# Performance work log

Measured on AMD Instinct MI355X. Metric: run time of the kernel, lower is better.

Reference implementation:

```python
import jax, jax.numpy as jnp
import numpy as np

HIDDEN = 1024
INTER = 4096
N_EXPERTS = 8
TOP_K = 2


def setup_inputs() -> dict:
    key = jax.random.key(0)
    ks = jax.random.split(key, 5)
    B, S = 2, 1024
    scale_h = 1.0 / np.sqrt(HIDDEN)
    scale_i = 1.0 / np.sqrt(INTER)
    return {
        "hidden_states": jax.random.normal(ks[0], (B, S, HIDDEN), dtype=jnp.float32),
        "router_w": jax.random.normal(ks[1], (N_EXPERTS, HIDDEN), dtype=jnp.float32) * scale_h,
        "gate_w": jax.random.normal(ks[2], (N_EXPERTS, INTER, HIDDEN), dtype=jnp.float32) * scale_h,
        "up_w": jax.random.normal(ks[3], (N_EXPERTS, INTER, HIDDEN), dtype=jnp.float32) * scale_h,
        "down_w": jax.random.normal(ks[4], (N_EXPERTS, HIDDEN, INTER), dtype=jnp.float32) * scale_i,
        "top_k": TOP_K,
    }


def reference(hidden_states, router_w, gate_w, up_w, down_w, top_k):
    B, S, D = hidden_states.shape
    E = router_w.shape[0]
    x = hidden_states.reshape(-1, D)              # [T, D]
    T = x.shape[0]

    router_logits = x @ router_w.T                # [T, E]
    probs = jax.nn.softmax(router_logits.astype(jnp.float32), axis=-1)
    routing_weights, selected = jax.lax.top_k(probs, top_k)   # [T, k]
    routing_weights = routing_weights.astype(x.dtype)

    # Dense combine weights: w[t, e] = routing weight if expert e selected for token t else 0
    combine = jnp.zeros((T, E), x.dtype).at[jnp.arange(T)[:, None], selected].add(routing_weights)

    # SwiGLU expert MLPs, computed for all experts then combined (same math as gather/scatter loop)
    g = jnp.einsum('td,ehd->eth', x, gate_w)      # [E, T, H]
    u = jnp.einsum('td,ehd->eth', x, up_w)        # [E, T, H]
    h = jax.nn.silu(g) * u
    expert_out = jnp.einsum('eth,edh->etd', h, down_w)  # [E, T, D]
    out = jnp.einsum('etd,te->td', expert_out, combine)  # [T, D]

    return out.reshape(B, S, D), router_logits
```

## Files before the change

### kernel.cpp

```cpp
#include <hip/hip_runtime.h>
#include <hip/hip_bf16.h>

#define HIDDEN 1024
#define INTER 4096
#define NEXP 8
#define T_TOK 2048

typedef short bf16x8 __attribute__((ext_vector_type(8)));
typedef float f32x4 __attribute__((ext_vector_type(4)));

__device__ __forceinline__ unsigned short f2bf(float f) {
    union { float f; unsigned int u; } v; v.f = f;
    unsigned int u = v.u;
    unsigned int r = (u + 0x7FFFu + ((u >> 16) & 1u)) >> 16;
    return (unsigned short)r;
}

__device__ __forceinline__ uint2 pack4trunc(float4 v) {
    union { float4 f; unsigned short s[8]; } u; u.f = v;
    uint2 r;
    r.x = (unsigned int)u.s[1] | ((unsigned int)u.s[3] << 16);
    r.y = (unsigned int)u.s[5] | ((unsigned int)u.s[7] << 16);
    return r;
}

__device__ __forceinline__ void block_sync() {
    asm volatile("s_waitcnt lgkmcnt(0)" ::: "memory");
    __builtin_amdgcn_s_barrier();
    asm volatile("" ::: "memory");
}

__global__ void router_kernel(const float* __restrict__ x,
                              const float* __restrict__ rw,
                              float* __restrict__ logits_out,
                              int* __restrict__ counts,
                              int* __restrict__ ids,
                              float* __restrict__ wts,
                              int* __restrict__ tsel) {
    int t = blockIdx.x * 4 + (threadIdx.x >> 6);
    int lane = threadIdx.x & 63;
    if (t >= T_TOK) return;
    const float4* xr = (const float4*)(x + (size_t)t * HIDDEN);
    float acc[NEXP];
#pragma unroll
    for (int e = 0; e < NEXP; e++) acc[e] = 0.f;
#pragma unroll
    for (int c = 0; c < 4; c++) {
        float4 xv = xr[lane + c * 64];
#pragma unroll
        for (int e = 0; e < NEXP; e++) {
            float4 wv = ((const float4*)(rw + (size_t)e * HIDDEN))[lane + c * 64];
            acc[e] += xv.x * wv.x + xv.y * wv.y + xv.z * wv.z + xv.w * wv.w;
        }
    }
#pragma unroll
    for (int e = 0; e < NEXP; e++) {
        float v = acc[e];
        for (int off = 32; off >= 1; off >>= 1) v += __shfl_xor(v, off, 64);
        acc[e] = v;
    }
    if (lane == 0) {
        float* lo = logits_out + (size_t)t * NEXP;
        float mx = acc[0];
#pragma unroll
        for (int e = 1; e < NEXP; e++) mx = fmaxf(mx, acc[e]);
        float p[NEXP], s = 0.f;
#pragma unroll
        for (int e = 0; e < NEXP; e++) { p[e] = __expf(acc[e] - mx); s += p[e]; }
        float inv = 1.f / s;
#pragma unroll
        for (int e = 0; e < NEXP; e++) { p[e] *= inv; lo[e] = acc[e]; }
        int i1 = 0;
#pragma unroll
        for (int e = 1; e < NEXP; e++) if (p[e] > p[i1]) i1 = e;
        int i2 = (i1 == 0) ? 1 : 0;
#pragma unroll
        for (int e = 0; e < NEXP; e++) if (e != i1 && e != i2 && p[e] > p[i2]) i2 = e;
        int s1 = atomicAdd(&counts[i1], 1);
        ids[i1 * T_TOK + s1] = t; wts[i1 * T_TOK + s1] = p[i1];
        int s2 = atomicAdd(&counts[i2], 1);
        ids[i2 * T_TOK + s2] = t; wts[i2 * T_TOK + s2] = p[i2];
        tsel[t * 2]     = i1 * T_TOK + s1;
        tsel[t * 2 + 1] = i2 * T_TOK + s2;
    }
}

__global__ void scan_kernel(const int* __restrict__ counts, int* __restrict__ offsets) {
    if (threadIdx.x == 0) {
        int s = 0;
        for (int e = 0; e < NEXP; e++) { offsets[e] = s; s += counts[e]; }
    }
}

__global__ __launch_bounds__(1024) void gemm_gu(
    const float* __restrict__ x, const float* __restrict__ gw, const float* __restrict__ uw,
    const int* __restrict__ counts, const int* __restrict__ offsets,
    const int* __restrict__ ids, unsigned short* __restrict__ h) {
    const int e = blockIdx.z;
    const int cnt = counts[e];
    const int mt = blockIdx.y;
    if (mt * 256 >= cnt) return;
    const int nt = blockIdx.x;
    const int tid = threadIdx.x;
    const int lane = tid & 63, wid = tid >> 6;
    const int wm = wid >> 2, wn = wid & 3;

    __shared__ __align__(16) char lds[65536];

    const float* gbase = gw + (size_t)e * INTER * HIDDEN;
    const float* ubase = uw + (size_t)e * INTER * HIDDEN;

    unsigned int aoff[2], wA[2];
#pragma unroll
    for (int j = 0; j < 2; j++) {
        int fi = j * 1024 + tid;
        int row = fi >> 3, c4 = fi & 7;
        int li = mt * 256 + row; if (li >= cnt) li = cnt - 1;
        int gid = ids[e * T_TOK + li];
        aoff[j] = (unsigned int)(gid * HIDDEN + c4 * 4);
        wA[j] = (unsigned int)((c4 >> 1) * 4096 + row * 16 + (c4 & 1) * 8);
    }
    unsigned int boff, wB;
    {
        int row = tid >> 3, c4 = tid & 7;
        boff = (unsigned int)((nt * 128 + row) * HIDDEN + c4 * 4);
        wB = (unsigned int)((c4 >> 1) * 2048 + row * 16 + (c4 & 1) * 8);
    }

    f32x4 accg[4][2], accu[4][2];
#pragma unroll
    for (int mf = 0; mf < 4; mf++)
#pragma unroll
        for (int nf = 0; nf < 2; nf++)
#pragma unroll
            for (int v = 0; v < 4; v++) { accg[mf][nf][v] = 0.f; accu[mf][nf][v] = 0.f; }

    float4 av[2], gv, uv;
    av[0] = *(const float4*)(x + aoff[0]);
    av[1] = *(const float4*)(x + aoff[1]);
    gv = *(const float4*)(gbase + boff);
    uv = *(const float4*)(ubase + boff);

    for (int kt = 0; kt < 32; kt++) {
        const unsigned int bb = (unsigned int)(kt & 1) << 15;
        *(uint2*)(lds + bb + wA[0]) = pack4trunc(av[0]);
        *(uint2*)(lds + bb + wA[1]) = pack4trunc(av[1]);
        *(uint2*)(lds + bb + 16384 + wB) = pack4trunc(gv);
        *(uint2*)(lds + bb + 24576 + wB) = pack4trunc(uv);
        if (kt < 31) {
            const int ko = (kt + 1) * 32;
            av[0] = *(const float4*)(x + aoff[0] + ko);
            av[1] = *(const float4*)(x + aoff[1] + ko);
            gv = *(const float4*)(gbase + boff + ko);
            uv = *(const float4*)(ubase + boff + ko);
        }
        block_sync();
        const unsigned int kq = (unsigned int)(lane >> 4);
        bf16x8 bg[2], bu[2];
#pragma unroll
        for (int nf = 0; nf < 2; nf++) {
            unsigned int rowb = (unsigned int)(wn * 32 + nf * 16 + (lane & 15));
            bg[nf] = *(const bf16x8*)(lds + bb + 16384 + kq * 2048 + rowb * 16);
            bu[nf] = *(const bf16x8*)(lds + bb + 24576 + kq * 2048 + rowb * 16);
        }
#pragma unroll
        for (int mf = 0; mf < 4; mf++) {
            unsigned int rowa = (unsigned int)(wm * 64 + mf * 16 + (lane & 15));
            bf16x8 a = *(const bf16x8*)(lds + bb + kq * 4096 + rowa * 16);
#pragma unroll
            for (int nf = 0; nf < 2; nf++) {
                accg[mf][nf] = __builtin_amdgcn_mfma_f32_16x16x32_bf16(a, bg[nf], accg[mf][nf], 0, 0, 0);
                accu[mf][nf] = __builtin_amdgcn_mfma_f32_16x16x32_bf16(a, bu[nf], accu[mf][nf], 0, 0, 0);
            }
        }
    }

    const int hoff = offsets[e];
#pragma unroll
    for (int mf = 0; mf < 4; mf++)
#pragma unroll
        for (int v = 0; v < 4; v++) {
            int il = wm * 64 + mf * 16 + ((lane >> 4) << 2) + v;
            int i = mt * 256 + il;
            if (i < cnt) {
                size_t rowbase = (size_t)(hoff + i) * INTER + nt * 128 + wn * 32 + (lane & 15);
#pragma unroll
                for (int nf = 0; nf < 2; nf++) {
                    float g = accg[mf][nf][v], u = accu[mf][nf][v];
                    float sg = g / (1.f + __expf(-g));
                    h[rowbase + nf * 16] = f2bf(sg * u);
                }
            }
        }
}

__global__ __launch_bounds__(512) void gemm_down(
    const unsigned short* __restrict__ h, const float* __restrict__ dw,
    const int* __restrict__ counts, const int* __restrict__ offsets,
    const float* __restrict__ wts, float* __restrict__ y) {
    const int ez = blockIdx.z;
    const int e = ez >> 1, ksp = ez & 1;
    const int cnt = counts[e];
    const int mt = blockIdx.y;
    if (mt * 128 >= cnt) return;
    const int nt = blockIdx.x;
    const int tid = threadIdx.x;
    const int lane = tid & 63, wid = tid >> 6;
    const int wm = wid >> 2, wn = wid & 3;

    __shared__ __align__(16) char lds[32768];

    const int hoff = offsets[e];
    const float* dbase = dw + (size_t)e * HIDDEN * INTER;

    unsigned int aoff, wAo;
    {
        int row = tid >> 2, c16 = tid & 3;
        int li = mt * 128 + row; if (li >= cnt) li = cnt - 1;
        aoff = (unsigned int)((hoff + li) * INTER + ksp * 2048 + c16 * 8);
        wAo = (unsigned int)(c16 * 2048 + row * 16);
    }
    unsigned int boff[2], wB[2];
#pragma unroll
    for (int j = 0; j < 2; j++) {
        int fi = j * 512 + tid;
        int row = fi >> 3, c4 = fi & 7;
        boff[j] = (unsigned int)((nt * 128 + row) * INTER + ksp * 2048 + c4 * 4);
        wB[j] = (unsigned int)(8192 + (c4 >> 1) * 2048 + row * 16 + (c4 & 1) * 8);
    }

    f32x4 acc[4][2];
#pragma unroll
    for (int mf = 0; mf < 4; mf++)
#pragma unroll
        for (int nf = 0; nf < 2; nf++)
#pragma unroll
            for (int v = 0; v < 4; v++) acc[mf][nf][v] = 0.f;

    int4 av; float4 bv[2];
    av = *(const int4*)(h + aoff);
    bv[0] = *(const float4*)(dbase + boff[0]);
    bv[1] = *(const float4*)(dbase + boff[1]);

    for (int kt = 0; kt < 64; kt++) {
        const unsigned int bb = (unsigned int)(kt & 1) << 14;
        *(int4*)(lds + bb + wAo) = av;
        *(uint2*)(lds + bb + wB[0]) = pack4trunc(bv[0]);
        *(uint2*)(lds + bb + wB[1]) = pack4trunc(bv[1]);
        if (kt < 63) {
            const int ko = (kt + 1) * 32;
            av = *(const int4*)(h + aoff + ko);
            bv[0] = *(const float4*)(dbase + boff[0] + ko);
            bv[1] = *(const float4*)(dbase + boff[1] + ko);
        }
        block_sync();
        const unsigned int kq = (unsigned int)(lane >> 4);
        bf16x8 bf[2];
#pragma unroll
        for (int nf = 0; nf < 2; nf++) {
            unsigned int rowb = (unsigned int)(wn * 32 + nf * 16 + (lane & 15));
            bf[nf] = *(const bf16x8*)(lds + bb + 8192 + kq * 2048 + rowb * 16);
        }
#pragma unroll
        for (int mf = 0; mf < 4; mf++) {
            unsigned int rowa = (unsigned int)(wm * 64 + mf * 16 + (lane & 15));
            bf16x8 a = *(const bf16x8*)(lds + bb + kq * 2048 + rowa * 16);
#pragma unroll
            for (int nf = 0; nf < 2; nf++)
                acc[mf][nf] = __builtin_amdgcn_mfma_f32_16x16x32_bf16(a, bf[nf], acc[mf][nf], 0, 0, 0);
        }
    }

#pragma unroll
    for (int mf = 0; mf < 4; mf++)
#pragma unroll
        for (int v = 0; v < 4; v++) {
            int il = wm * 64 + mf * 16 + ((lane >> 4) << 2) + v;
            int i = mt * 128 + il;
            if (i < cnt) {
                float w = wts[e * T_TOK + i];
                float* yrow = y + ((size_t)ksp * 4096 + hoff + i) * HIDDEN
                                + nt * 128 + wn * 32 + (lane & 15);
#pragma unroll
                for (int nf = 0; nf < 2; nf++)
                    yrow[nf * 16] = w * acc[mf][nf][v];
            }
        }
}

__global__ __launch_bounds__(256) void combine_kernel(
    const float* __restrict__ y, const int* __restrict__ offsets,
    const int* __restrict__ tsel, float* __restrict__ out) {
    const int t = blockIdx.x;
    const int d = threadIdx.x * 4;
    int p0 = tsel[t * 2], p1 = tsel[t * 2 + 1];
    size_t g0 = (size_t)(offsets[p0 >> 11] + (p0 & (T_TOK - 1)));
    size_t g1 = (size_t)(offsets[p1 >> 11] + (p1 & (T_TOK - 1)));
    float4 a0 = *(const float4*)(y + g0 * HIDDEN + d);
    float4 a1 = *(const float4*)(y + (4096 + g0) * HIDDEN + d);
    float4 b0 = *(const float4*)(y + g1 * HIDDEN + d);
    float4 b1 = *(const float4*)(y + (4096 + g1) * HIDDEN + d);
    float4 o;
    o.x = (a0.x + a1.x) + (b0.x + b1.x);
    o.y = (a0.y + a1.y) + (b0.y + b1.y);
    o.z = (a0.z + a1.z) + (b0.z + b1.z);
    o.w = (a0.w + a1.w) + (b0.w + b1.w);
    *(float4*)(out + (size_t)t * HIDDEN + d) = o;
}

extern "C" void kernel_launch(void* const* d_in, const int* in_sizes, int n_in,
                              void* d_out, int out_size, void* d_ws, size_t ws_size,
                              hipStream_t stream) {
    const float* x  = (const float*)d_in[0];
    const float* rw = (const float*)d_in[1];
    const float* gw = (const float*)d_in[2];
    const float* uw = (const float*)d_in[3];
    const float* dw = (const float*)d_in[4];
    float* out = (float*)d_out;
    float* logits = out + (size_t)T_TOK * HIDDEN;

    char* ws = (char*)d_ws;
    int*   counts  = (int*)ws;
    int*   offsets = (int*)(ws + 32);
    int*   tsel    = (int*)(ws + 1024);
    int*   ids     = (int*)(ws + 20480);
    float* wts     = (float*)(ws + 90112);
    unsigned short* h = (unsigned short*)(ws + 262144);
    float* y       = (float*)(ws + 262144 + 33554432);

    hipMemsetAsync(counts, 0, 8 * sizeof(int), stream);

    router_kernel<<<T_TOK / 4, 256, 0, stream>>>(x, rw, logits, counts, ids, wts, tsel);
    scan_kernel<<<1, 64, 0, stream>>>(counts, offsets);
    gemm_gu<<<dim3(INTER / 128, 8, NEXP), 1024, 0, stream>>>(x, gw, uw, counts, offsets, ids, h);
    gemm_down<<<dim3(HIDDEN / 128, 16, NEXP * 2), 512, 0, stream>>>(h, dw, counts, offsets, wts, y);
    combine_kernel<<<T_TOK, 256, 0, stream>>>(y, offsets, tsel, out);
}
```

Before: 293.7 us.

## Retile expert GEMMs with XOR-swizzled LDS, smaller blocks and swapped grid order

Shrinks gemm_gu to 128-row M tiles with 512 threads and gemm_down to 256 threads with a 64-wide per-wave N tile, so each wave does more MFMAs per LDS fragment load. LDS layout becomes row-major 64-byte rows with an XOR swizzle on the k-chunk to avoid bank conflicts, with 16-byte packed stores. The grid puts the token-tile index in x so blocks that share weight tiles are scheduled near each other, and launch bounds ask for higher occupancy. The h output now truncates to bf16 instead of rounding, which slightly changes numerics.

```diff
diff --git a/kernel.cpp b/kernel.cpp
--- a/kernel.cpp
+++ b/kernel.cpp
@@ -9,18 +9,20 @@
 typedef short bf16x8 __attribute__((ext_vector_type(8)));
 typedef float f32x4 __attribute__((ext_vector_type(4)));
 
+#define CHUNK(row, kq) ((unsigned int)((row) * 64u + ((((unsigned int)(kq)) ^ ((((unsigned int)(row)) >> 1) & 3u)) << 4)))
+
 __device__ __forceinline__ unsigned short f2bf(float f) {
     union { float f; unsigned int u; } v; v.f = f;
-    unsigned int u = v.u;
-    unsigned int r = (u + 0x7FFFu + ((u >> 16) & 1u)) >> 16;
-    return (unsigned short)r;
-}
-
-__device__ __forceinline__ uint2 pack4trunc(float4 v) {
-    union { float4 f; unsigned short s[8]; } u; u.f = v;
-    uint2 r;
-    r.x = (unsigned int)u.s[1] | ((unsigned int)u.s[3] << 16);
-    r.y = (unsigned int)u.s[5] | ((unsigned int)u.s[7] << 16);
+    return (unsigned short)(v.u >> 16);
+}
+
+__device__ __forceinline__ uint4 pack8trunc(float4 a, float4 b) {
+    union { float4 f; unsigned short s[8]; } x, y; x.f = a; y.f = b;
+    uint4 r;
+    r.x = (unsigned int)x.s[1] | ((unsigned int)x.s[3] << 16);
+    r.y = (unsigned int)x.s[5] | ((unsigned int)x.s[7] << 16);
+    r.z = (unsigned int)y.s[1] | ((unsigned int)y.s[3] << 16);
+    r.w = (unsigned int)y.s[5] | ((unsigned int)y.s[7] << 16);
     return r;
 }
 
@@ -92,40 +94,30 @@
     }
 }
 
-__global__ __launch_bounds__(1024) void gemm_gu(
+__global__ __launch_bounds__(512, 4) void gemm_gu(
     const float* __restrict__ x, const float* __restrict__ gw, const float* __restrict__ uw,
     const int* __restrict__ counts, const int* __restrict__ offsets,
     const int* __restrict__ ids, unsigned short* __restrict__ h) {
     const int e = blockIdx.z;
     const int cnt = counts[e];
-    const int mt = blockIdx.y;
-    if (mt * 256 >= cnt) return;
-    const int nt = blockIdx.x;
+    const int mt = blockIdx.x;
+    if (mt * 128 >= cnt) return;
+    const int nt = blockIdx.y;
     const int tid = threadIdx.x;
     const int lane = tid & 63, wid = tid >> 6;
     const int wm = wid >> 2, wn = wid & 3;
 
-    __shared__ __align__(16) char lds[65536];
+    __shared__ __align__(16) char lds[49152];
 
     const float* gbase = gw + (size_t)e * INTER * HIDDEN;
     const float* ubase = uw + (size_t)e * INTER * HIDDEN;
 
-    unsigned int aoff[2], wA[2];
-#pragma unroll
-    for (int j = 0; j < 2; j++) {
-        int fi = j * 1024 + tid;
-        int row = fi >> 3, c4 = fi & 7;
-        int li = mt * 256 + row; if (li >= cnt) li = cnt - 1;
-        int gid = ids[e * T_TOK + li];
-        aoff[j] = (unsigned int)(gid * HIDDEN + c4 * 4);
-        wA[j] = (unsigned int)((c4 >> 1) * 4096 + row * 16 + (c4 & 1) * 8);
-    }
-    unsigned int boff, wB;
-    {
-        int row = tid >> 3, c4 = tid & 7;
-        boff = (unsigned int)((nt * 128 + row) * HIDDEN + c4 * 4);
-        wB = (unsigned int)((c4 >> 1) * 2048 + row * 16 + (c4 & 1) * 8);
-    }
+    const int arow = tid >> 2, akq = tid & 3;
+    int ali = mt * 128 + arow; if (ali >= cnt) ali = cnt - 1;
+    const unsigned int aoff = (unsigned int)(ids[e * T_TOK + ali] * HIDDEN + akq * 8);
+    const unsigned int wAo = CHUNK(arow, akq);
+    const unsigned int boff = (unsigned int)((nt * 128 + arow) * HIDDEN + akq * 8);
+    const unsigned int wBo = CHUNK(arow, akq);
 
     f32x4 accg[4][2], accu[4][2];
 #pragma unroll
@@ -135,42 +127,38 @@
 #pragma unroll
             for (int v = 0; v < 4; v++) { accg[mf][nf][v] = 0.f; accu[mf][nf][v] = 0.f; }
 
-    float4 av[2], gv, uv;
-    av[0] = *(const float4*)(x + aoff[0]);
-    av[1] = *(const float4*)(x + aoff[1]);
-    gv = *(const float4*)(gbase + boff);
-    uv = *(const float4*)(ubase + boff);
+    float4 a0, a1, g0, g1, u0, u1;
+    a0 = *(const float4*)(x + aoff);     a1 = *(const float4*)(x + aoff + 4);
+    g0 = *(const float4*)(gbase + boff); g1 = *(const float4*)(gbase + boff + 4);
+    u0 = *(const float4*)(ubase + boff); u1 = *(const float4*)(ubase + boff + 4);
 
     for (int kt = 0; kt < 32; kt++) {
-        const unsigned int bb = (unsigned int)(kt & 1) << 15;
-        *(uint2*)(lds + bb + wA[0]) = pack4trunc(av[0]);
-        *(uint2*)(lds + bb + wA[1]) = pack4trunc(av[1]);
-        *(uint2*)(lds + bb + 16384 + wB) = pack4trunc(gv);
-        *(uint2*)(lds + bb + 24576 + wB) = pack4trunc(uv);
+        const unsigned int bb = (unsigned int)(kt & 1) * 24576u;
+        *(uint4*)(lds + bb + wAo) = pack8trunc(a0, a1);
+        *(uint4*)(lds + bb + 8192 + wBo) = pack8trunc(g0, g1);
+        *(uint4*)(lds + bb + 16384 + wBo) = pack8trunc(u0, u1);
         if (kt < 31) {
             const int ko = (kt + 1) * 32;
-            av[0] = *(const float4*)(x + aoff[0] + ko);
-            av[1] = *(const float4*)(x + aoff[1] + ko);
-            gv = *(const float4*)(gbase + boff + ko);
-            uv = *(const float4*)(ubase + boff + ko);
+            a0 = *(const float4*)(x + aoff + ko);     a1 = *(const float4*)(x + aoff + ko + 4);
+            g0 = *(const float4*)(gbase + boff + ko); g1 = *(const float4*)(gbase + boff + ko + 4);
+            u0 = *(const float4*)(ubase + boff + ko); u1 = *(const float4*)(ubase + boff + ko + 4);
         }
         block_sync();
-        const unsigned int kq = (unsigned int)(lane >> 4);
-        bf16x8 bg[2], bu[2];
+        const unsigned int kqr = (unsigned int)(lane >> 4);
+        const unsigned int rl = (unsigned int)(lane & 15);
+        bf16x8 a[4];
+#pragma unroll
+        for (int mf = 0; mf < 4; mf++)
+            a[mf] = *(const bf16x8*)(lds + bb + CHUNK(wm * 64 + mf * 16 + rl, kqr));
 #pragma unroll
         for (int nf = 0; nf < 2; nf++) {
-            unsigned int rowb = (unsigned int)(wn * 32 + nf * 16 + (lane & 15));
-            bg[nf] = *(const bf16x8*)(lds + bb + 16384 + kq * 2048 + rowb * 16);
-            bu[nf] = *(const bf16x8*)(lds + bb + 24576 + kq * 2048 + rowb * 16);
-        }
-#pragma unroll
-        for (int mf = 0; mf < 4; mf++) {
-            unsigned int rowa = (unsigned int)(wm * 64 + mf * 16 + (lane & 15));
-            bf16x8 a = *(const bf16x8*)(lds + bb + kq * 4096 + rowa * 16);
-#pragma unroll
-            for (int nf = 0; nf < 2; nf++) {
-                accg[mf][nf] = __builtin_amdgcn_mfma_f32_16x16x32_bf16(a, bg[nf], accg[mf][nf], 0, 0, 0);
-                accu[mf][nf] = __builtin_amdgcn_mfma_f32_16x16x32_bf16(a, bu[nf], accu[mf][nf], 0, 0, 0);
+            const unsigned int brow = wn * 32 + nf * 16 + rl;
+            bf16x8 bg = *(const bf16x8*)(lds + bb + 8192 + CHUNK(brow, kqr));
+            bf16x8 bu = *(const bf16x8*)(lds + bb + 16384 + CHUNK(brow, kqr));
+#pragma unroll
+            for (int mf = 0; mf < 4; mf++) {
+                accg[mf][nf] = __builtin_amdgcn_mfma_f32_16x16x32_bf16(a[mf], bg, accg[mf][nf], 0, 0, 0);
+                accu[mf][nf] = __builtin_amdgcn_mfma_f32_16x16x32_bf16(a[mf], bu, accu[mf][nf], 0, 0, 0);
             }
         }
     }
@@ -181,7 +169,7 @@
 #pragma unroll
         for (int v = 0; v < 4; v++) {
             int il = wm * 64 + mf * 16 + ((lane >> 4) << 2) + v;
-            int i = mt * 256 + il;
+            int i = mt * 128 + il;
             if (i < cnt) {
                 size_t rowbase = (size_t)(hoff + i) * INTER + nt * 128 + wn * 32 + (lane & 15);
 #pragma unroll
@@ -194,80 +182,88 @@
         }
 }
 
-__global__ __launch_bounds__(512) void gemm_down(
+__global__ __launch_bounds__(256, 4) void gemm_down(
     const unsigned short* __restrict__ h, const float* __restrict__ dw,
     const int* __restrict__ counts, const int* __restrict__ offsets,
     const float* __restrict__ wts, float* __restrict__ y) {
     const int ez = blockIdx.z;
     const int e = ez >> 1, ksp = ez & 1;
     const int cnt = counts[e];
-    const int mt = blockIdx.y;
+    const int mt = blockIdx.x;
     if (mt * 128 >= cnt) return;
-    const int nt = blockIdx.x;
+    const int nt = blockIdx.y;
     const int tid = threadIdx.x;
     const int lane = tid & 63, wid = tid >> 6;
-    const int wm = wid >> 2, wn = wid & 3;
+    const int wm = wid >> 1, wn = wid & 1;
 
     __shared__ __align__(16) char lds[32768];
 
     const int hoff = offsets[e];
     const float* dbase = dw + (size_t)e * HIDDEN * INTER;
 
-    unsigned int aoff, wAo;
-    {
-        int row = tid >> 2, c16 = tid & 3;
+    unsigned int aoff[2], wA[2];
+#pragma unroll
+    for (int j = 0; j < 2; j++) {
+        int fi = j * 256 + tid;
+        int row = fi >> 2, kq = fi & 3;
         int li = mt * 128 + row; if (li >= cnt) li = cnt - 1;
-        aoff = (unsigned int)((hoff + li) * INTER + ksp * 2048 + c16 * 8);
-        wAo = (unsigned int)(c16 * 2048 + row * 16);
+        aoff[j] = (unsigned int)((hoff + li) * INTER + ksp * 2048 + kq * 8);
+        wA[j] = CHUNK(row, kq);
     }
     unsigned int boff[2], wB[2];
 #pragma unroll
     for (int j = 0; j < 2; j++) {
-        int fi = j * 512 + tid;
-        int row = fi >> 3, c4 = fi & 7;
-        boff[j] = (unsigned int)((nt * 128 + row) * INTER + ksp * 2048 + c4 * 4);
-        wB[j] = (unsigned int)(8192 + (c4 >> 1) * 2048 + row * 16 + (c4 & 1) * 8);
-    }
-
-    f32x4 acc[4][2];
+        int fi = j * 256 + tid;
+        int row = fi >> 2, kq = fi & 3;
+        boff[j] = (unsigned int)((nt * 128 + row) * INTER + ksp * 2048 + kq * 8);
+        wB[j] = 8192u + CHUNK(row, kq);
+    }
+
+    f32x4 acc[4][4];
 #pragma unroll
     for (int mf = 0; mf < 4; mf++)
 #pragma unroll
-        for (int nf = 0; nf < 2; nf++)
+        for (int nf = 0; nf < 4; nf++)
 #pragma unroll
             for (int v = 0; v < 4; v++) acc[mf][nf][v] = 0.f;
 
-    int4 av; float4 bv[2];
-    av = *(const int4*)(h + aoff);
-    bv[0] = *(const float4*)(dbase + boff[0]);
-    bv[1] = *(const float4*)(dbase + boff[1]);
+    int4 av[2]; float4 bv0[2], bv1[2];
+#pragma unroll
+    for (int j = 0; j < 2; j++) {
+        av[j] = *(const int4*)(h + aoff[j]);
+        bv0[j] = *(const float4*)(dbase + boff[j]);
+        bv1[j] = *(const float4*)(dbase + boff[j] + 4);
+    }
 
     for (int kt = 0; kt < 64; kt++) {
         const unsigned int bb = (unsigned int)(kt & 1) << 14;
-        *(int4*)(lds + bb + wAo) = av;
-        *(uint2*)(lds + bb + wB[0]) = pack4trunc(bv[0]);
-        *(uint2*)(lds + bb + wB[1]) = pack4trunc(bv[1]);
+#pragma unroll
+        for (int j = 0; j < 2; j++) {
+            *(int4*)(lds + bb + wA[j]) = av[j];
+            *(uint4*)(lds + bb + wB[j]) = pack8trunc(bv0[j], bv1[j]);
+        }
         if (kt < 63) {
             const int ko = (kt + 1) * 32;
-            av = *(const int4*)(h + aoff + ko);
-            bv[0] = *(const float4*)(dbase + boff[0] + ko);
-            bv[1] = *(const float4*)(dbase + boff[1] + ko);
+#pragma unroll
+            for (int j = 0; j < 2; j++) {
+                av[j] = *(const int4*)(h + aoff[j] + ko);
+                bv0[j] = *(const float4*)(dbase + boff[j] + ko);
+                bv1[j] = *(const float4*)(dbase + boff[j] + ko + 4);
+            }
         }
         block_sync();
-        const unsigned int kq = (unsigned int)(lane >> 4);
-        bf16x8 bf[2];
-#pragma unroll
-        for (int nf = 0; nf < 2; nf++) {
-            unsigned int rowb = (unsigned int)(wn * 32 + nf * 16 + (lane & 15));
-            bf[nf] = *(const bf16x8*)(lds + bb + 8192 + kq * 2048 + rowb * 16);
-        }
-#pragma unroll
-        for (int mf = 0; mf < 4; mf++) {
-            unsigned int rowa = (unsigned int)(wm * 64 + mf * 16 + (lane & 15));
-            bf16x8 a = *(const bf16x8*)(lds + bb + kq * 2048 + rowa * 16);
-#pragma unroll
-            for (int nf = 0; nf < 2; nf++)
-                acc[mf][nf] = __builtin_amdgcn_mfma_f32_16x16x32_bf16(a, bf[nf], acc[mf][nf], 0, 0, 0);
+        const unsigned int kqr = (unsigned int)(lane >> 4);
+        const unsigned int rl = (unsigned int)(lane & 15);
+        bf16x8 a[4];
+#pragma unroll
+        for (int mf = 0; mf < 4; mf++)
+            a[mf] = *(const bf16x8*)(lds + bb + CHUNK(wm * 64 + mf * 16 + rl, kqr));
+#pragma unroll
+        for (int nf = 0; nf < 4; nf++) {
+            bf16x8 b = *(const bf16x8*)(lds + bb + 8192 + CHUNK(wn * 64 + nf * 16 + rl, kqr));
+#pragma unroll
+            for (int mf = 0; mf < 4; mf++)
+                acc[mf][nf] = __builtin_amdgcn_mfma_f32_16x16x32_bf16(a[mf], b, acc[mf][nf], 0, 0, 0);
         }
     }
 
@@ -280,9 +276,9 @@
             if (i < cnt) {
                 float w = wts[e * T_TOK + i];
                 float* yrow = y + ((size_t)ksp * 4096 + hoff + i) * HIDDEN
-                                + nt * 128 + wn * 32 + (lane & 15);
-#pragma unroll
-                for (int nf = 0; nf < 2; nf++)
+                                + nt * 128 + wn * 64 + (lane & 15);
+#pragma unroll
+                for (int nf = 0; nf < 4; nf++)
                     yrow[nf * 16] = w * acc[mf][nf][v];
             }
         }
@@ -332,7 +328,7 @@
 
     router_kernel<<<T_TOK / 4, 256, 0, stream>>>(x, rw, logits, counts, ids, wts, tsel);
     scan_kernel<<<1, 64, 0, stream>>>(counts, offsets);
-    gemm_gu<<<dim3(INTER / 128, 8, NEXP), 1024, 0, stream>>>(x, gw, uw, counts, offsets, ids, h);
-    gemm_down<<<dim3(HIDDEN / 128, 16, NEXP * 2), 512, 0, stream>>>(h, dw, counts, offsets, wts, y);
+    gemm_gu<<<dim3(16, INTER / 128, NEXP), 512, 0, stream>>>(x, gw, uw, counts, offsets, ids, h);
+    gemm_down<<<dim3(16, HIDDEN / 128, NEXP * 2), 256, 0, stream>>>(h, dw, counts, offsets, wts, y);
     combine_kernel<<<T_TOK, 256, 0, stream>>>(y, offsets, tsel, out);
 }
```

Result: slower. 881.2 us (+200.1%).

## Deepen GEMM prefetch to two stages with XOR-swizzled LDS and 16B stores

Applied to the files above, without the earlier changes.

Both expert GEMM kernels now hold two K-tiles of global loads in flight, using explicit even/odd register sets and LDS buffers instead of a single prefetched tile. The LDS layout changes to row-major 64-byte rows with an XOR swizzle on the k-chunk to avoid bank conflicts. Each thread now packs and writes eight bf16 values in one 16-byte store rather than two 8-byte stores, and gate/up loading is split across the two halves of the block. The f2bf conversion for h switches from round-to-nearest to truncation, which is cheaper but changes numerics slightly, and register pressure rises with the extra prefetch buffers.

```diff
diff --git a/kernel.cpp b/kernel.cpp
--- a/kernel.cpp
+++ b/kernel.cpp
@@ -9,18 +9,20 @@
 typedef short bf16x8 __attribute__((ext_vector_type(8)));
 typedef float f32x4 __attribute__((ext_vector_type(4)));
 
+#define CHUNK(row, kq) ((unsigned int)((row) * 64u + ((((unsigned int)(kq)) ^ ((((unsigned int)(row)) >> 1) & 3u)) << 4)))
+
 __device__ __forceinline__ unsigned short f2bf(float f) {
     union { float f; unsigned int u; } v; v.f = f;
-    unsigned int u = v.u;
-    unsigned int r = (u + 0x7FFFu + ((u >> 16) & 1u)) >> 16;
-    return (unsigned short)r;
-}
-
-__device__ __forceinline__ uint2 pack4trunc(float4 v) {
-    union { float4 f; unsigned short s[8]; } u; u.f = v;
-    uint2 r;
-    r.x = (unsigned int)u.s[1] | ((unsigned int)u.s[3] << 16);
-    r.y = (unsigned int)u.s[5] | ((unsigned int)u.s[7] << 16);
+    return (unsigned short)(v.u >> 16);
+}
+
+__device__ __forceinline__ uint4 pack8trunc(float4 a, float4 b) {
+    union { float4 f; unsigned short s[8]; } x, y; x.f = a; y.f = b;
+    uint4 r;
+    r.x = (unsigned int)x.s[1] | ((unsigned int)x.s[3] << 16);
+    r.y = (unsigned int)x.s[5] | ((unsigned int)x.s[7] << 16);
+    r.z = (unsigned int)y.s[1] | ((unsigned int)y.s[3] << 16);
+    r.w = (unsigned int)y.s[5] | ((unsigned int)y.s[7] << 16);
     return r;
 }
 
@@ -107,25 +109,16 @@
 
     __shared__ __align__(16) char lds[65536];
 
-    const float* gbase = gw + (size_t)e * INTER * HIDDEN;
-    const float* ubase = uw + (size_t)e * INTER * HIDDEN;
-
-    unsigned int aoff[2], wA[2];
-#pragma unroll
-    for (int j = 0; j < 2; j++) {
-        int fi = j * 1024 + tid;
-        int row = fi >> 3, c4 = fi & 7;
-        int li = mt * 256 + row; if (li >= cnt) li = cnt - 1;
-        int gid = ids[e * T_TOK + li];
-        aoff[j] = (unsigned int)(gid * HIDDEN + c4 * 4);
-        wA[j] = (unsigned int)((c4 >> 1) * 4096 + row * 16 + (c4 & 1) * 8);
-    }
-    unsigned int boff, wB;
-    {
-        int row = tid >> 3, c4 = tid & 7;
-        boff = (unsigned int)((nt * 128 + row) * HIDDEN + c4 * 4);
-        wB = (unsigned int)((c4 >> 1) * 2048 + row * 16 + (c4 & 1) * 8);
-    }
+    const int arow = tid >> 2, akq = tid & 3;
+    int ali = mt * 256 + arow; if (ali >= cnt) ali = cnt - 1;
+    const unsigned int aoff = (unsigned int)(ids[e * T_TOK + ali] * HIDDEN + akq * 8);
+    const unsigned int wAo = CHUNK(arow, akq);
+    const int bsel = tid >> 9;
+    const int bi = tid & 511;
+    const int brow = bi >> 2, bkq = bi & 3;
+    const float* bsrc = (bsel ? uw : gw) + (size_t)e * INTER * HIDDEN
+                        + (size_t)(nt * 128 + brow) * HIDDEN + bkq * 8;
+    const unsigned int wBo = 16384u + ((unsigned int)bsel << 13) + CHUNK(brow, bkq);
 
     f32x4 accg[4][2], accu[4][2];
 #pragma unroll
@@ -135,45 +128,54 @@
 #pragma unroll
             for (int v = 0; v < 4; v++) { accg[mf][nf][v] = 0.f; accu[mf][nf][v] = 0.f; }
 
-    float4 av[2], gv, uv;
-    av[0] = *(const float4*)(x + aoff[0]);
-    av[1] = *(const float4*)(x + aoff[1]);
-    gv = *(const float4*)(gbase + boff);
-    uv = *(const float4*)(ubase + boff);
-
-    for (int kt = 0; kt < 32; kt++) {
-        const unsigned int bb = (unsigned int)(kt & 1) << 15;
-        *(uint2*)(lds + bb + wA[0]) = pack4trunc(av[0]);
-        *(uint2*)(lds + bb + wA[1]) = pack4trunc(av[1]);
-        *(uint2*)(lds + bb + 16384 + wB) = pack4trunc(gv);
-        *(uint2*)(lds + bb + 24576 + wB) = pack4trunc(uv);
-        if (kt < 31) {
-            const int ko = (kt + 1) * 32;
-            av[0] = *(const float4*)(x + aoff[0] + ko);
-            av[1] = *(const float4*)(x + aoff[1] + ko);
-            gv = *(const float4*)(gbase + boff + ko);
-            uv = *(const float4*)(ubase + boff + ko);
+    float4 aE0, aE1, bE0, bE1, aO0, aO1, bO0, bO1;
+    aE0 = *(const float4*)(x + aoff);      aE1 = *(const float4*)(x + aoff + 4);
+    bE0 = *(const float4*)(bsrc);          bE1 = *(const float4*)(bsrc + 4);
+    aO0 = *(const float4*)(x + aoff + 32); aO1 = *(const float4*)(x + aoff + 36);
+    bO0 = *(const float4*)(bsrc + 32);     bO1 = *(const float4*)(bsrc + 36);
+
+#define GU_COMPUTE(BB)                                                                  \
+    {                                                                                   \
+        const unsigned int kqr = (unsigned int)(lane >> 4);                             \
+        const unsigned int rl = (unsigned int)(lane & 15);                              \
+        bf16x8 a[4];                                                                    \
+        _Pragma("unroll")                                                               \
+        for (int mf = 0; mf < 4; mf++)                                                  \
+            a[mf] = *(const bf16x8*)(lds + (BB) + CHUNK(wm * 64 + mf * 16 + rl, kqr));  \
+        _Pragma("unroll")                                                               \
+        for (int nf = 0; nf < 2; nf++) {                                                \
+            const unsigned int br = wn * 32 + nf * 16 + rl;                             \
+            bf16x8 bg = *(const bf16x8*)(lds + (BB) + 16384 + CHUNK(br, kqr));          \
+            bf16x8 bu = *(const bf16x8*)(lds + (BB) + 24576 + CHUNK(br, kqr));          \
+            _Pragma("unroll")                                                           \
+            for (int mf = 0; mf < 4; mf++) {                                            \
+                accg[mf][nf] = __builtin_amdgcn_mfma_f32_16x16x32_bf16(a[mf], bg, accg[mf][nf], 0, 0, 0); \
+                accu[mf][nf] = __builtin_amdgcn_mfma_f32_16x16x32_bf16(a[mf], bu, accu[mf][nf], 0, 0, 0); \
+            }                                                                           \
+        }                                                                               \
+    }
+
+    for (int kt = 0; kt < 32; kt += 2) {
+        *(uint4*)(lds + wAo) = pack8trunc(aE0, aE1);
+        *(uint4*)(lds + wBo) = pack8trunc(bE0, bE1);
+        if (kt + 2 < 32) {
+            const int ko = (kt + 2) * 32;
+            aE0 = *(const float4*)(x + aoff + ko); aE1 = *(const float4*)(x + aoff + ko + 4);
+            bE0 = *(const float4*)(bsrc + ko);     bE1 = *(const float4*)(bsrc + ko + 4);
         }
         block_sync();
-        const unsigned int kq = (unsigned int)(lane >> 4);
-        bf16x8 bg[2], bu[2];
-#pragma unroll
-        for (int nf = 0; nf < 2; nf++) {
-            unsigned int rowb = (unsigned int)(wn * 32 + nf * 16 + (lane & 15));
-            bg[nf] = *(const bf16x8*)(lds + bb + 16384 + kq * 2048 + rowb * 16);
-            bu[nf] = *(const bf16x8*)(lds + bb + 24576 + kq * 2048 + rowb * 16);
-        }
-#pragma unroll
-        for (int mf = 0; mf < 4; mf++) {
-            unsigned int rowa = (unsigned int)(wm * 64 + mf * 16 + (lane & 15));
-            bf16x8 a = *(const bf16x8*)(lds + bb + kq * 4096 + rowa * 16);
-#pragma unroll
-            for (int nf = 0; nf < 2; nf++) {
-                accg[mf][nf] = __builtin_amdgcn_mfma_f32_16x16x32_bf16(a, bg[nf], accg[mf][nf], 0, 0, 0);
-                accu[mf][nf] = __builtin_amdgcn_mfma_f32_16x16x32_bf16(a, bu[nf], accu[mf][nf], 0, 0, 0);
-            }
-        }
-    }
+        GU_COMPUTE(0u)
+        *(uint4*)(lds + 32768 + wAo) = pack8trunc(aO0, aO1);
+        *(uint4*)(lds + 32768 + wBo) = pack8trunc(bO0, bO1);
+        if (kt + 3 < 32) {
+            const int ko = (kt + 3) * 32;
+            aO0 = *(const float4*)(x + aoff + ko); aO1 = *(const float4*)(x + aoff + ko + 4);
+            bO0 = *(const float4*)(bsrc + ko);     bO1 = *(const float4*)(bsrc + ko + 4);
+        }
+        block_sync();
+        GU_COMPUTE(32768u)
+    }
+#undef GU_COMPUTE
 
     const int hoff = offsets[e];
 #pragma unroll
@@ -213,21 +215,12 @@
     const int hoff = offsets[e];
     const float* dbase = dw + (size_t)e * HIDDEN * INTER;
 
-    unsigned int aoff, wAo;
-    {
-        int row = tid >> 2, c16 = tid & 3;
-        int li = mt * 128 + row; if (li >= cnt) li = cnt - 1;
-        aoff = (unsigned int)((hoff + li) * INTER + ksp * 2048 + c16 * 8);
-        wAo = (unsigned int)(c16 * 2048 + row * 16);
-    }
-    unsigned int boff[2], wB[2];
-#pragma unroll
-    for (int j = 0; j < 2; j++) {
-        int fi = j * 512 + tid;
-        int row = fi >> 3, c4 = fi & 7;
-        boff[j] = (unsigned int)((nt * 128 + row) * INTER + ksp * 2048 + c4 * 4);
-        wB[j] = (unsigned int)(8192 + (c4 >> 1) * 2048 + row * 16 + (c4 & 1) * 8);
-    }
+    const int row = tid >> 2, kq = tid & 3;
+    int li = mt * 128 + row; if (li >= cnt) li = cnt - 1;
+    const unsigned int aoff = (unsigned int)((hoff + li) * INTER + ksp * 2048 + kq * 8);
+    const unsigned int wAo = CHUNK(row, kq);
+    const unsigned int boff = (unsigned int)((nt * 128 + row) * INTER + ksp * 2048 + kq * 8);
+    const unsigned int wBo = 8192u + CHUNK(row, kq);
 
     f32x4 acc[4][2];
 #pragma unroll
@@ -237,39 +230,50 @@
 #pragma unroll
             for (int v = 0; v < 4; v++) acc[mf][nf][v] = 0.f;
 
-    int4 av; float4 bv[2];
-    av = *(const int4*)(h + aoff);
-    bv[0] = *(const float4*)(dbase + boff[0]);
-    bv[1] = *(const float4*)(dbase + boff[1]);
-
-    for (int kt = 0; kt < 64; kt++) {
-        const unsigned int bb = (unsigned int)(kt & 1) << 14;
-        *(int4*)(lds + bb + wAo) = av;
-        *(uint2*)(lds + bb + wB[0]) = pack4trunc(bv[0]);
-        *(uint2*)(lds + bb + wB[1]) = pack4trunc(bv[1]);
-        if (kt < 63) {
-            const int ko = (kt + 1) * 32;
-            av = *(const int4*)(h + aoff + ko);
-            bv[0] = *(const float4*)(dbase + boff[0] + ko);
-            bv[1] = *(const float4*)(dbase + boff[1] + ko);
+    int4 avE, avO; float4 bE0, bE1, bO0, bO1;
+    avE = *(const int4*)(h + aoff);
+    bE0 = *(const float4*)(dbase + boff);      bE1 = *(const float4*)(dbase + boff + 4);
+    avO = *(const int4*)(h + aoff + 32);
+    bO0 = *(const float4*)(dbase + boff + 32); bO1 = *(const float4*)(dbase + boff + 36);
+
+#define DN_COMPUTE(BB)                                                                  \
+    {                                                                                   \
+        const unsigned int kqr = (unsigned int)(lane >> 4);                             \
+        const unsigned int rl = (unsigned int)(lane & 15);                              \
+        bf16x8 a[4];                                                                    \
+        _Pragma("unroll")                                                               \
+        for (int mf = 0; mf < 4; mf++)                                                  \
+            a[mf] = *(const bf16x8*)(lds + (BB) + CHUNK(wm * 64 + mf * 16 + rl, kqr));  \
+        _Pragma("unroll")                                                               \
+        for (int nf = 0; nf < 2; nf++) {                                                \
+            bf16x8 b = *(const bf16x8*)(lds + (BB) + 8192 + CHUNK(wn * 32 + nf * 16 + rl, kqr)); \
+            _Pragma("unroll")                                                           \
+            for (int mf = 0; mf < 4; mf++)                                              \
+                acc[mf][nf] = __builtin_amdgcn_mfma_f32_16x16x32_bf16(a[mf], b, acc[mf][nf], 0, 0, 0); \
+        }                                                                               \
+    }
+
+    for (int kt = 0; kt < 64; kt += 2) {
+        *(int4*)(lds + wAo) = avE;
+        *(uint4*)(lds + wBo) = pack8trunc(bE0, bE1);
+        if (kt + 2 < 64) {
+            const int ko = (kt + 2) * 32;
+            avE = *(const int4*)(h + aoff + ko);
+            bE0 = *(const float4*)(dbase + boff + ko); bE1 = *(const float4*)(dbase + boff + ko + 4);
         }
         block_sync();
-        const unsigned int kq = (unsigned int)(lane >> 4);
-        bf16x8 bf[2];
-#pragma unroll
-        for (int nf = 0; nf < 2; nf++) {
-            unsigned int rowb = (unsigned int)(wn * 32 + nf * 16 + (lane & 15));
-            bf[nf] = *(const bf16x8*)(lds + bb + 8192 + kq * 2048 + rowb * 16);
-        }
-#pragma unroll
-        for (int mf = 0; mf < 4; mf++) {
-            unsigned int rowa = (unsigned int)(wm * 64 + mf * 16 + (lane & 15));
-            bf16x8 a = *(const bf16x8*)(lds + bb + kq * 2048 + rowa * 16);
-#pragma unroll
-            for (int nf = 0; nf < 2; nf++)
-                acc[mf][nf] = __builtin_amdgcn_mfma_f32_16x16x32_bf16(a, bf[nf], acc[mf][nf], 0, 0, 0);
-        }
-    }
+        DN_COMPUTE(0u)
+        *(int4*)(lds + 16384 + wAo) = avO;
+        *(uint4*)(lds + 16384 + wBo) = pack8trunc(bO0, bO1);
+        if (kt + 3 < 64) {
+            const int ko = (kt + 3) * 32;
+            avO = *(const int4*)(h + aoff + ko);
+            bO0 = *(const float4*)(dbase + boff + ko); bO1 = *(const float4*)(dbase + boff + ko + 4);
+        }
+        block_sync();
+        DN_COMPUTE(16384u)
+    }
+#undef DN_COMPUTE
 
 #pragma unroll
     for (int mf = 0; mf < 4; mf++)
```

Measured after the change: 358.0 us. 1.22x slower.
